# Kernel tuning notes

Hardware: AMD Instinct MI355X
Metric: run time of the kernel (lower is better)

Reference implementation:

```python
import jax, jax.numpy as jnp
import numpy as np

K = 30  # hardcoded top-k in take_top_k_dropout(x, 30, ...)


def _topk_channel_mask(x, k):
    # x: [B, C, H, W]; binary mask with 1 at the top-k |x| channels per pixel.
    B, C, H, W = x.shape
    xa = jnp.abs(x).reshape(B, C, H * W).transpose(0, 2, 1).reshape(B * H * W, C)
    _, idx = jax.lax.top_k(xa, k)  # [BHW, k]
    rows = jnp.arange(B * H * W)[:, None]
    mask = jnp.zeros((B * H * W, C), x.dtype).at[rows, idx].set(1.0)
    return mask.reshape(B, H * W, C).transpose(0, 2, 1).reshape(B, C, H, W)


def _saturation(z, phi, jump):
    # Saturation_activation_per_filter.forward
    l1 = (jnp.sum(jnp.abs(phi), axis=0) + 1e-12).reshape(1, -1, 1, 1)  # [1,C,1,1]
    r = z / l1
    r = 0.5 * (jnp.sign(r - jump) + jnp.sign(r + jump))
    return r * l1


def _conv_transpose(x, w, b, stride):
    # PyTorch ConvTranspose2d(padding=0): w is [in, out, kh, kw]
    k = w.shape[-1]
    wt = jnp.flip(w, (2, 3)).transpose(1, 0, 2, 3)  # -> [out, in, kh, kw]
    y = jax.lax.conv_general_dilated(
        x, wt, window_strides=(1, 1),
        padding=[(k - 1, k - 1), (k - 1, k - 1)],
        lhs_dilation=(stride, stride),
        dimension_numbers=('NCHW', 'OIHW', 'NCHW'))
    return y + b.reshape(1, -1, 1, 1)


def _take_middle(x):
    width = x.shape[-1]
    s = (width - 32) // 2
    return x[:, :, s:s + 32, s:s + 32]


def setup_inputs() -> dict:
    key = jax.random.key(0)
    ks = jax.random.split(key, 9)
    B, C, H, W, D = 128, 500, 16, 16, 192
    return {
        'x': jax.random.normal(ks[0], (B, C, H, W), jnp.float32),
        'phi': jax.random.normal(ks[1], (D, C), jnp.float32),
        'jump': jnp.float32(0.1),
        'w1': jax.random.normal(ks[2], (C, 300, 4, 4), jnp.float32) * 0.02,
        'b1': jax.random.normal(ks[3], (300,), jnp.float32) * 0.02,
        'w2': jax.random.normal(ks[4], (300, 100, 3, 3), jnp.float32) * 0.02,
        'b2': jax.random.normal(ks[5], (100,), jnp.float32) * 0.02,
        'w3': jax.random.normal(ks[6], (100, 3, 3, 3), jnp.float32) * 0.02,
        'b3': jax.random.normal(ks[7], (3,), jnp.float32) * 0.02,
    }


def reference(x, phi, jump, w1, b1, w2, b2, w3, b3):
    # eval mode: dropout(ones) == ones, no training rescalings
    out = x * _topk_channel_mask(x, K)
    out = _saturation(out, phi, jump)
    out = jax.nn.relu(_conv_transpose(out, w1, b1, 2))
    out = jax.nn.relu(_conv_transpose(out, w2, b2, 1))
    out = jax.nn.relu(_conv_transpose(out, w3, b3, 1))
    return _take_middle(out)
```

## Files before the change

kernel.cpp:

```cpp
#include <hip/hip_runtime.h>
#include <stdint.h>

#define B_   128
#define C_   500
#define H_   16
#define P_   256
#define D_   192
#define C1O  300
#define H1   34
#define P1   (H1*H1)
#define C2O  100
#define H2   36
#define P2   (H2*H2)
#define C3O  3
#define H3   38
#define P3   (H3*H3)
#define CROP 3
#define OW_  32
#define KTOP 30

#define NSCAN  1000
#define NL1B   16
#define NTABB  25
#define NPAIR  (B_ * C_)

__device__ __forceinline__ float sgnf(float v){ return (v > 0.f) ? 1.f : ((v < 0.f) ? -1.f : 0.f); }

__device__ __forceinline__ int pat36(int i){
  if (i == 0) return 0;
  if (i == 1) return 1;
  if (i <= 33) return 2;
  if (i == 34) return 3;
  return 4;
}

__global__ __launch_bounds__(256) void k_pre(
    const float* __restrict__ x, const float* __restrict__ phi,
    const float* __restrict__ jumpp, const float* __restrict__ b1,
    const float* __restrict__ w2, const float* __restrict__ b2,
    const float* __restrict__ w3,
    float* __restrict__ l1, float* __restrict__ thr,
    float* __restrict__ tab, float* __restrict__ part,
    float* __restrict__ M){
  const int blk = blockIdx.x;
  const int t = threadIdx.x;
  const int wave = t >> 6, lane = t & 63;

  if (blk < NSCAN){
    const int g = blk * 4 + wave;
    const float* xg = x + (size_t)g * 16 * P_ + lane * 4;
#pragma unroll
    for (int j0 = 0; j0 < 16; j0 += 4){
      float4 v0 = *(const float4*)(xg + (size_t)(j0 + 0) * P_);
      float4 v1 = *(const float4*)(xg + (size_t)(j0 + 1) * P_);
      float4 v2 = *(const float4*)(xg + (size_t)(j0 + 2) * P_);
      float4 v3 = *(const float4*)(xg + (size_t)(j0 + 3) * P_);
      float m0 = fmaxf(fmaxf(fabsf(v0.x), fabsf(v0.y)), fmaxf(fabsf(v0.z), fabsf(v0.w)));
      float m1 = fmaxf(fmaxf(fabsf(v1.x), fabsf(v1.y)), fmaxf(fabsf(v1.z), fabsf(v1.w)));
      float m2 = fmaxf(fmaxf(fabsf(v2.x), fabsf(v2.y)), fmaxf(fabsf(v2.z), fabsf(v2.w)));
      float m3 = fmaxf(fmaxf(fabsf(v3.x), fabsf(v3.y)), fmaxf(fabsf(v3.z), fabsf(v3.w)));
#pragma unroll
      for (int off = 32; off; off >>= 1){
        m0 = fmaxf(m0, __shfl_down(m0, off));
        m1 = fmaxf(m1, __shfl_down(m1, off));
        m2 = fmaxf(m2, __shfl_down(m2, off));
        m3 = fmaxf(m3, __shfl_down(m3, off));
      }
      if (lane == 0)
        *(float4*)(M + g * 16 + j0) = make_float4(m0, m1, m2, m3);
    }
    return;
  }

  if (blk < NSCAN + NL1B){
    __shared__ float red[8][32];
    const int bb = blk - NSCAN;
    const int cl = t & 31, dg = t >> 5;
    const int c = bb * 32 + cl;
    float s = 0.f;
    if (c < C_){
      const int d0 = dg * 24;
#pragma unroll 4
      for (int d = d0; d < d0 + 24; ++d) s += fabsf(phi[d * C_ + c]);
    }
    red[dg][cl] = s;
    __syncthreads();
    if (t < 32){
      int cc = bb * 32 + t;
      if (cc < C_){
        float sum = 1e-12f;
#pragma unroll
        for (int g = 0; g < 8; ++g) sum += red[g][t];
        l1[cc] = sum;
        thr[cc] = jumpp[0] * sum;
      }
    }
    return;
  }

  const int k = blk - (NSCAN + NL1B);
  const int o = k * 4 + wave;
  __shared__ float S[4][9];
  __shared__ float tabR[4][25];
  __shared__ float w3s[4][27];

  for (int i = t; i < 4 * 27; i += 256) w3s[i / 27][i % 27] = w3[(k * 4 + i / 27) * 27 + i % 27];

  {
    float acc[9] = {0,0,0,0,0,0,0,0,0};
    for (int c1 = lane; c1 < C1O; c1 += 64){
      float a1 = fmaxf(b1[c1], 0.f);
      const float* w = w2 + (c1 * C2O + o) * 9;
#pragma unroll
      for (int tap = 0; tap < 9; ++tap) acc[tap] += w[tap] * a1;
    }
#pragma unroll
    for (int tap = 0; tap < 9; ++tap)
      for (int off = 32; off; off >>= 1) acc[tap] += __shfl_down(acc[tap], off);
    if (lane == 0){
#pragma unroll
      for (int tap = 0; tap < 9; ++tap) S[wave][tap] = acc[tap];
    }
  }
  __syncthreads();

  if (lane < 25){
    const int lo5[5] = {0,0,0,1,2}, hi5[5] = {0,1,2,2,2};
    int pr = lane / 5, pc = lane % 5;
    float s = b2[o];
    for (int kh = lo5[pr]; kh <= hi5[pr]; ++kh)
      for (int kw = lo5[pc]; kw <= hi5[pc]; ++kw) s += S[wave][kh * 3 + kw];
    tab[o * 25 + lane] = s;
    tabR[wave][lane] = s;
  }
  __syncthreads();

  for (int pp = 0; pp < 4; ++pp){
    const int pos = pp * 256 + t;
    const int r = pos >> 5, cc = pos & 31;
    const int oh = r + CROP, ow = cc + CROP;
    int ph[3], pw[3];
#pragma unroll
    for (int kk = 0; kk < 3; ++kk){ ph[kk] = pat36(oh - kk); pw[kk] = pat36(ow - kk); }
    float a0 = 0.f, a1v = 0.f, a2v = 0.f;
#pragma unroll
    for (int j = 0; j < 4; ++j){
      const float* tc = tabR[j];
      const float* wc = w3s[j];
#pragma unroll
      for (int kh = 0; kh < 3; ++kh){
        const int prr = ph[kh] * 5;
#pragma unroll
        for (int kw = 0; kw < 3; ++kw){
          float a2 = fmaxf(tc[prr + pw[kw]], 0.f);
          a0  += wc[0 * 9 + kh * 3 + kw] * a2;
          a1v += wc[1 * 9 + kh * 3 + kw] * a2;
          a2v += wc[2 * 9 + kh * 3 + kw] * a2;
        }
      }
    }
    part[(k * 3 + 0) * 1024 + pos] = a0;
    part[(k * 3 + 1) * 1024 + pos] = a1v;
    part[(k * 3 + 2) * 1024 + pos] = a2v;
  }
}

__global__ void k_final(const float* __restrict__ x, const float* __restrict__ l1,
                        const float* __restrict__ jumpp, const float* __restrict__ tab,
                        const float* __restrict__ w1, const float* __restrict__ b1,
                        const float* __restrict__ w2, const float* __restrict__ w3,
                        const float* __restrict__ b3v,
                        const float* __restrict__ part, const float* __restrict__ M,
                        const float* __restrict__ thr,
                        signed char* __restrict__ zq, float* __restrict__ u1,
                        float* __restrict__ u2, float* __restrict__ out, int have){
  const int b = blockIdx.x;
  const int t = threadIdx.x;
  const int wave = t >> 6, lane = t & 63;

  __shared__ unsigned char hot[P_];
  __shared__ unsigned char um[256];
  __shared__ unsigned char d1s[P1];
  __shared__ unsigned char d2s[P2];
  __shared__ int s_any;
  __shared__ float sx[C_];
  __shared__ unsigned char rm[C_];
  __shared__ unsigned long long red[4];
  __shared__ int sel[KTOP];

  if (t == 0) s_any = 0;
  __syncthreads();
  for (int c = t; c < C_; c += 256)
    if (M[b * C_ + c] >= thr[c]) s_any = 1;
  __syncthreads();

  if (!s_any){
    for (int i = t; i < 3 * OW_ * (OW_ / 4); i += 256){
      int o = i >> 8, rr = i & 255;
      int r = rr >> 3, q4 = rr & 7;
      int pos = r * 32 + q4 * 4;
      float bv = b3v[o];
      float4 s = make_float4(bv, bv, bv, bv);
      for (int k = 0; k < NTABB; ++k){
        const float4 v = *(const float4*)(part + ((size_t)(k * 3 + o) << 10) + pos);
        s.x += v.x; s.y += v.y; s.z += v.z; s.w += v.w;
      }
      float4 res;
      res.x = fmaxf(s.x, 0.f);
      res.y = fmaxf(s.y, 0.f);
      res.z = fmaxf(s.z, 0.f);
      res.w = fmaxf(s.w, 0.f);
      *(float4*)(out + ((size_t)(b * 3 + o) * OW_ + r) * OW_ + q4 * 4) = res;
    }
    return;
  }
  if (!have) return;

  {
    const int q = t & 15, cg = t >> 4;
    for (int tile = 0; tile < 4; ++tile){
      unsigned m = 0;
      const int pbase = tile * 64 + 4 * q;
      for (int c = cg; c < C_; c += 16){
        float tc = thr[c];
        const float4 v = *(const float4*)(x + ((size_t)(b * C_ + c)) * P_ + pbase);
        if (fabsf(v.x) >= tc) m |= 1u;
        if (fabsf(v.y) >= tc) m |= 2u;
        if (fabsf(v.z) >= tc) m |= 4u;
        if (fabsf(v.w) >= tc) m |= 8u;
      }
      um[t] = (unsigned char)m;
      __syncthreads();
      if (t < 64){
        const int qq = t >> 2, j = t & 3;
        unsigned mm = 0;
#pragma unroll
        for (int g = 0; g < 16; ++g) mm |= um[g * 16 + qq];
        hot[tile * 64 + t] = (unsigned char)((mm >> j) & 1u);
      }
      __syncthreads();
    }
  }

  const float J = jumpp[0];

  for (int px = 0; px < P_; ++px){
    if (!hot[px]) continue;
    for (int c = t; c < C_; c += 256){ sx[c] = x[(b * C_ + c) * P_ + px]; rm[c] = 0; }
    __syncthreads();
    for (int it = 0; it < KTOP; ++it){
      unsigned long long best = 0ULL;
      for (int c = t; c < C_; c += 256){
        if (!rm[c]){
          unsigned long long key =
            ((unsigned long long)__float_as_uint(fabsf(sx[c])) << 32) |
            (unsigned int)(C_ - 1 - c);
          if (key > best) best = key;
        }
      }
      for (int off = 32; off; off >>= 1){
        unsigned long long o2 = __shfl_down(best, off);
        if (o2 > best) best = o2;
      }
      if ((t & 63) == 0) red[t >> 6] = best;
      __syncthreads();
      if (t == 0){
        unsigned long long mx = red[0];
        for (int wv = 1; wv < 4; ++wv) if (red[wv] > mx) mx = red[wv];
        int idx = C_ - 1 - (int)(mx & 0xffffffffULL);
        sel[it] = idx;
        rm[idx] = 1;
      }
      __syncthreads();
    }
    for (int c = t; c < C_; c += 256) zq[(b * C_ + c) * P_ + px] = 0;
    __syncthreads();
    if (t < KTOP){
      int c = sel[t];
      float r = sx[c] / l1[c];
      float qv = 0.5f * (sgnf(r - J) + sgnf(r + J));
      int code = (int)(2.f * qv);
      if (code) zq[(b * C_ + c) * P_ + px] = (signed char)code;
    }
    __syncthreads();
  }

  for (int p1 = t; p1 < P1; p1 += 256){
    int ih = p1 / H1, iw = p1 - (p1 / H1) * H1;
    int h0 = max(0, (ih - 2) >> 1), h1v = min(H_ - 1, ih >> 1);
    int w0 = max(0, (iw - 2) >> 1), w1v = min(H_ - 1, iw >> 1);
    int any = 0;
    for (int h = h0; h <= h1v; ++h)
      for (int w = w0; w <= w1v; ++w)
        any |= hot[h * H_ + w];
    d1s[p1] = (unsigned char)(any != 0);
  }
  __syncthreads();

  for (int p2 = t; p2 < P2; p2 += 256){
    int oh = p2 / H2, ow = p2 - (p2 / H2) * H2;
    int any = 0;
    for (int kh = 0; kh < 3; ++kh){
      int ih = oh - kh; if (ih < 0 || ih >= H1) continue;
      for (int kw = 0; kw < 3; ++kw){
        int iw = ow - kw; if (iw < 0 || iw >= H1) continue;
        any |= d1s[ih * H1 + iw];
      }
    }
    d2s[p2] = (unsigned char)(any != 0);
  }
  __syncthreads();

  for (int p1 = wave; p1 < P1; p1 += 4){
    if (!d1s[p1]) continue;
    int ih = p1 / H1, iw = p1 - (p1 / H1) * H1;
    float acc[5] = {0,0,0,0,0};
    int h0 = max(0, (ih - 2) >> 1), h1v = min(H_ - 1, ih >> 1);
    int w0 = max(0, (iw - 2) >> 1), w1v = min(H_ - 1, iw >> 1);
    for (int h = h0; h <= h1v; ++h)
      for (int w = w0; w <= w1v; ++w){
        if (!hot[h * H_ + w]) continue;
        int kh = ih - 2 * h, kw = iw - 2 * w;
        const signed char* zp = zq + (size_t)(b * C_) * P_ + h * H_ + w;
        for (int c = 0; c < C_; ++c){
          int code = zp[(size_t)c * P_];
          if (!code) continue;
          float val = 0.5f * (float)code * l1[c];
          const float* wp = w1 + (size_t)(c * C1O) * 16 + kh * 4 + kw;
#pragma unroll
          for (int j = 0; j < 5; ++j){
            int c1 = j * 64 + lane;
            if (c1 < C1O) acc[j] += wp[(size_t)c1 * 16] * val;
          }
        }
      }
#pragma unroll
    for (int j = 0; j < 5; ++j){
      int c1 = j * 64 + lane;
      if (c1 < C1O){
        float bb = b1[c1];
        u1[(size_t)(b * C1O + c1) * P1 + p1] = fmaxf(bb + acc[j], 0.f) - fmaxf(bb, 0.f);
      }
    }
  }
  __syncthreads();

  for (int p2 = wave; p2 < P2; p2 += 4){
    if (!d2s[p2]) continue;
    int oh = p2 / H2, ow = p2 - (p2 / H2) * H2;
    float acc[2] = {0,0};
    for (int kh = 0; kh < 3; ++kh){
      int ih = oh - kh; if (ih < 0 || ih >= H1) continue;
      for (int kw = 0; kw < 3; ++kw){
        int iw = ow - kw; if (iw < 0 || iw >= H1) continue;
        if (!d1s[ih * H1 + iw]) continue;
        const float* up = u1 + (size_t)(b * C1O) * P1 + ih * H1 + iw;
        const float* wb = w2 + kh * 3 + kw;
        for (int c1 = 0; c1 < C1O; ++c1){
          float uv = up[(size_t)c1 * P1];
          if (uv == 0.f) continue;
          const float* wp = wb + (size_t)(c1 * C2O) * 9;
#pragma unroll
          for (int j = 0; j < 2; ++j){
            int c2 = j * 64 + lane;
            if (c2 < C2O) acc[j] += wp[(size_t)c2 * 9] * uv;
          }
        }
      }
    }
    int pr = pat36(oh) * 5 + pat36(ow);
#pragma unroll
    for (int j = 0; j < 2; ++j){
      int c2 = j * 64 + lane;
      if (c2 < C2O){
        float bs = tab[c2 * 25 + pr];
        u2[(size_t)(b * C2O + c2) * P2 + p2] = fmaxf(bs + acc[j], 0.f) - fmaxf(bs, 0.f);
      }
    }
  }
  __syncthreads();

  for (int i = t; i < 3 * OW_ * OW_; i += 256){
    int o = i >> 10, rc = i & 1023;
    int r = rc >> 5, cc = rc & 31;
    int oh = r + CROP, ow = cc + CROP;
    float acc = b3v[o];
    for (int k = 0; k < NTABB; ++k) acc += part[((size_t)(k * 3 + o) << 10) + rc];
    for (int kh = 0; kh < 3; ++kh){
      int ih = oh - kh;
      for (int kw = 0; kw < 3; ++kw){
        int iw = ow - kw;
        if (!d2s[ih * H2 + iw]) continue;
        const float* up = u2 + (size_t)(b * C2O) * P2 + ih * H2 + iw;
        const float* wp = w3 + o * 9 + kh * 3 + kw;
        for (int c2 = 0; c2 < C2O; ++c2){
          float uv = up[(size_t)c2 * P2];
          if (uv != 0.f) acc += wp[c2 * 27] * uv;
        }
      }
    }
    out[((size_t)(b * 3 + o) * OW_ + r) * OW_ + cc] = fmaxf(acc, 0.f);
  }
}

extern "C" void kernel_launch(void* const* d_in, const int* in_sizes, int n_in,
                              void* d_out, int out_size, void* d_ws, size_t ws_size,
                              hipStream_t stream){
  const float* x   = (const float*)d_in[0];
  const float* phi = (const float*)d_in[1];
  const float* jmp = (const float*)d_in[2];
  const float* w1  = (const float*)d_in[3];
  const float* b1  = (const float*)d_in[4];
  const float* w2  = (const float*)d_in[5];
  const float* b2  = (const float*)d_in[6];
  const float* w3  = (const float*)d_in[7];
  const float* b3  = (const float*)d_in[8];
  float* out = (float*)d_out;
  char* ws = (char*)d_ws;

  constexpr size_t OFF_L1   = 0;
  constexpr size_t OFF_THR  = OFF_L1   + 2048;
  constexpr size_t OFF_TAB  = OFF_THR  + 2048;
  constexpr size_t OFF_PART = OFF_TAB  + 10240;
  constexpr size_t OFF_M    = OFF_PART + (size_t)NTABB * 3 * 1024 * 4;
  constexpr size_t OFF_ZQ   = OFF_M    + (size_t)NPAIR * 4;
  constexpr size_t OFF_U1   = OFF_ZQ   + (size_t)B_ * C_ * P_;
  constexpr size_t OFF_U2   = OFF_U1   + (size_t)B_ * C1O * P1 * 4;
  constexpr size_t TOTAL    = OFF_U2   + (size_t)B_ * C2O * P2 * 4;

  float* l1p  = (float*)(ws + OFF_L1);
  float* thrp = (float*)(ws + OFF_THR);
  float* tabp = (float*)(ws + OFF_TAB);
  float* prtp = (float*)(ws + OFF_PART);
  float* Mp   = (float*)(ws + OFF_M);
  signed char* zqp = (signed char*)(ws + OFF_ZQ);
  float* u1p = (float*)(ws + OFF_U1);
  float* u2p = (float*)(ws + OFF_U2);
  int have = (ws_size >= TOTAL) ? 1 : 0;

  k_pre  <<<NSCAN + NL1B + NTABB, 256, 0, stream>>>(x, phi, jmp, b1, w2, b2, w3,
                                                    l1p, thrp, tabp, prtp, Mp);
  k_final<<<B_, 256, 0, stream>>>(x, l1p, jmp, tabp, w1, b1, w2, w3, b3,
                                  prtp, Mp, thrp, zqp, u1p, u2p, out, have);
}
```

Before: 118.5 us.

## Fuse precompute and final kernels into one cooperative launch with grid sync

```diff
diff --git a/kernel.cpp b/kernel.cpp
--- a/kernel.cpp
+++ b/kernel.cpp
@@ -1,5 +1,8 @@
 #include <hip/hip_runtime.h>
+#include <hip/hip_cooperative_groups.h>
 #include <stdint.h>
+
+namespace cg = cooperative_groups;
 
 #define B_   128
 #define C_   500
@@ -22,6 +25,7 @@
 #define NSCAN  1000
 #define NL1B   16
 #define NTABB  25
+#define NGRID  (NSCAN + NL1B + NTABB)
 #define NPAIR  (B_ * C_)
 
 __device__ __forceinline__ float sgnf(float v){ return (v > 0.f) ? 1.f : ((v < 0.f) ? -1.f : 0.f); }
@@ -34,150 +38,26 @@
   return 4;
 }
 
-__global__ __launch_bounds__(256) void k_pre(
+__global__ __launch_bounds__(256, 5) void k_all(
     const float* __restrict__ x, const float* __restrict__ phi,
     const float* __restrict__ jumpp, const float* __restrict__ b1,
     const float* __restrict__ w2, const float* __restrict__ b2,
-    const float* __restrict__ w3,
+    const float* __restrict__ w3, const float* __restrict__ b3v,
+    const float* __restrict__ w1,
     float* __restrict__ l1, float* __restrict__ thr,
     float* __restrict__ tab, float* __restrict__ part,
-    float* __restrict__ M){
+    float* __restrict__ M,
+    signed char* __restrict__ zq, float* __restrict__ u1,
+    float* __restrict__ u2, float* __restrict__ out,
+    int have, int mode){
   const int blk = blockIdx.x;
   const int t = threadIdx.x;
   const int wave = t >> 6, lane = t & 63;
 
-  if (blk < NSCAN){
-    const int g = blk * 4 + wave;
-    const float* xg = x + (size_t)g * 16 * P_ + lane * 4;
-#pragma unroll
-    for (int j0 = 0; j0 < 16; j0 += 4){
-      float4 v0 = *(const float4*)(xg + (size_t)(j0 + 0) * P_);
-      float4 v1 = *(const float4*)(xg + (size_t)(j0 + 1) * P_);
-      float4 v2 = *(const float4*)(xg + (size_t)(j0 + 2) * P_);
-      float4 v3 = *(const float4*)(xg + (size_t)(j0 + 3) * P_);
-      float m0 = fmaxf(fmaxf(fabsf(v0.x), fabsf(v0.y)), fmaxf(fabsf(v0.z), fabsf(v0.w)));
-      float m1 = fmaxf(fmaxf(fabsf(v1.x), fabsf(v1.y)), fmaxf(fabsf(v1.z), fabsf(v1.w)));
-      float m2 = fmaxf(fmaxf(fabsf(v2.x), fabsf(v2.y)), fmaxf(fabsf(v2.z), fabsf(v2.w)));
-      float m3 = fmaxf(fmaxf(fabsf(v3.x), fabsf(v3.y)), fmaxf(fabsf(v3.z), fabsf(v3.w)));
-#pragma unroll
-      for (int off = 32; off; off >>= 1){
-        m0 = fmaxf(m0, __shfl_down(m0, off));
-        m1 = fmaxf(m1, __shfl_down(m1, off));
-        m2 = fmaxf(m2, __shfl_down(m2, off));
-        m3 = fmaxf(m3, __shfl_down(m3, off));
-      }
-      if (lane == 0)
-        *(float4*)(M + g * 16 + j0) = make_float4(m0, m1, m2, m3);
-    }
-    return;
-  }
-
-  if (blk < NSCAN + NL1B){
-    __shared__ float red[8][32];
-    const int bb = blk - NSCAN;
-    const int cl = t & 31, dg = t >> 5;
-    const int c = bb * 32 + cl;
-    float s = 0.f;
-    if (c < C_){
-      const int d0 = dg * 24;
-#pragma unroll 4
-      for (int d = d0; d < d0 + 24; ++d) s += fabsf(phi[d * C_ + c]);
-    }
-    red[dg][cl] = s;
-    __syncthreads();
-    if (t < 32){
-      int cc = bb * 32 + t;
-      if (cc < C_){
-        float sum = 1e-12f;
-#pragma unroll
-        for (int g = 0; g < 8; ++g) sum += red[g][t];
-        l1[cc] = sum;
-        thr[cc] = jumpp[0] * sum;
-      }
-    }
-    return;
-  }
-
-  const int k = blk - (NSCAN + NL1B);
-  const int o = k * 4 + wave;
-  __shared__ float S[4][9];
+  __shared__ float redf[8][32];
+  __shared__ float S4[4][9];
   __shared__ float tabR[4][25];
-  __shared__ float w3s[4][27];
-
-  for (int i = t; i < 4 * 27; i += 256) w3s[i / 27][i % 27] = w3[(k * 4 + i / 27) * 27 + i % 27];
-
-  {
-    float acc[9] = {0,0,0,0,0,0,0,0,0};
-    for (int c1 = lane; c1 < C1O; c1 += 64){
-      float a1 = fmaxf(b1[c1], 0.f);
-      const float* w = w2 + (c1 * C2O + o) * 9;
-#pragma unroll
-      for (int tap = 0; tap < 9; ++tap) acc[tap] += w[tap] * a1;
-    }
-#pragma unroll
-    for (int tap = 0; tap < 9; ++tap)
-      for (int off = 32; off; off >>= 1) acc[tap] += __shfl_down(acc[tap], off);
-    if (lane == 0){
-#pragma unroll
-      for (int tap = 0; tap < 9; ++tap) S[wave][tap] = acc[tap];
-    }
-  }
-  __syncthreads();
-
-  if (lane < 25){
-    const int lo5[5] = {0,0,0,1,2}, hi5[5] = {0,1,2,2,2};
-    int pr = lane / 5, pc = lane % 5;
-    float s = b2[o];
-    for (int kh = lo5[pr]; kh <= hi5[pr]; ++kh)
-      for (int kw = lo5[pc]; kw <= hi5[pc]; ++kw) s += S[wave][kh * 3 + kw];
-    tab[o * 25 + lane] = s;
-    tabR[wave][lane] = s;
-  }
-  __syncthreads();
-
-  for (int pp = 0; pp < 4; ++pp){
-    const int pos = pp * 256 + t;
-    const int r = pos >> 5, cc = pos & 31;
-    const int oh = r + CROP, ow = cc + CROP;
-    int ph[3], pw[3];
-#pragma unroll
-    for (int kk = 0; kk < 3; ++kk){ ph[kk] = pat36(oh - kk); pw[kk] = pat36(ow - kk); }
-    float a0 = 0.f, a1v = 0.f, a2v = 0.f;
-#pragma unroll
-    for (int j = 0; j < 4; ++j){
-      const float* tc = tabR[j];
-      const float* wc = w3s[j];
-#pragma unroll
-      for (int kh = 0; kh < 3; ++kh){
-        const int prr = ph[kh] * 5;
-#pragma unroll
-        for (int kw = 0; kw < 3; ++kw){
-          float a2 = fmaxf(tc[prr + pw[kw]], 0.f);
-          a0  += wc[0 * 9 + kh * 3 + kw] * a2;
-          a1v += wc[1 * 9 + kh * 3 + kw] * a2;
-          a2v += wc[2 * 9 + kh * 3 + kw] * a2;
-        }
-      }
-    }
-    part[(k * 3 + 0) * 1024 + pos] = a0;
-    part[(k * 3 + 1) * 1024 + pos] = a1v;
-    part[(k * 3 + 2) * 1024 + pos] = a2v;
-  }
-}
-
-__global__ void k_final(const float* __restrict__ x, const float* __restrict__ l1,
-                        const float* __restrict__ jumpp, const float* __restrict__ tab,
-                        const float* __restrict__ w1, const float* __restrict__ b1,
-                        const float* __restrict__ w2, const float* __restrict__ w3,
-                        const float* __restrict__ b3v,
-                        const float* __restrict__ part, const float* __restrict__ M,
-                        const float* __restrict__ thr,
-                        signed char* __restrict__ zq, float* __restrict__ u1,
-                        float* __restrict__ u2, float* __restrict__ out, int have){
-  const int b = blockIdx.x;
-  const int t = threadIdx.x;
-  const int wave = t >> 6, lane = t & 63;
-
+  __shared__ float w3s4[4][27];
   __shared__ unsigned char hot[P_];
   __shared__ unsigned char um[256];
   __shared__ unsigned char d1s[P1];
@@ -185,8 +65,126 @@
   __shared__ int s_any;
   __shared__ float sx[C_];
   __shared__ unsigned char rm[C_];
-  __shared__ unsigned long long red[4];
+  __shared__ unsigned long long redu[4];
   __shared__ int sel[KTOP];
+
+  if (mode != 2){
+    if (blk < NSCAN){
+      const int g = blk * 4 + wave;
+      const float* xg = x + (size_t)g * 16 * P_ + lane * 4;
+#pragma unroll
+      for (int j0 = 0; j0 < 16; j0 += 4){
+        float4 v0 = *(const float4*)(xg + (size_t)(j0 + 0) * P_);
+        float4 v1 = *(const float4*)(xg + (size_t)(j0 + 1) * P_);
+        float4 v2 = *(const float4*)(xg + (size_t)(j0 + 2) * P_);
+        float4 v3 = *(const float4*)(xg + (size_t)(j0 + 3) * P_);
+        float m0 = fmaxf(fmaxf(fabsf(v0.x), fabsf(v0.y)), fmaxf(fabsf(v0.z), fabsf(v0.w)));
+        float m1 = fmaxf(fmaxf(fabsf(v1.x), fabsf(v1.y)), fmaxf(fabsf(v1.z), fabsf(v1.w)));
+        float m2 = fmaxf(fmaxf(fabsf(v2.x), fabsf(v2.y)), fmaxf(fabsf(v2.z), fabsf(v2.w)));
+        float m3 = fmaxf(fmaxf(fabsf(v3.x), fabsf(v3.y)), fmaxf(fabsf(v3.z), fabsf(v3.w)));
+#pragma unroll
+        for (int off = 32; off; off >>= 1){
+          m0 = fmaxf(m0, __shfl_down(m0, off));
+          m1 = fmaxf(m1, __shfl_down(m1, off));
+          m2 = fmaxf(m2, __shfl_down(m2, off));
+          m3 = fmaxf(m3, __shfl_down(m3, off));
+        }
+        if (lane == 0)
+          *(float4*)(M + g * 16 + j0) = make_float4(m0, m1, m2, m3);
+      }
+    } else if (blk < NSCAN + NL1B){
+      const int bb = blk - NSCAN;
+      const int cl = t & 31, dg = t >> 5;
+      const int c = bb * 32 + cl;
+      float s = 0.f;
+      if (c < C_){
+        const int d0 = dg * 24;
+#pragma unroll 4
+        for (int d = d0; d < d0 + 24; ++d) s += fabsf(phi[d * C_ + c]);
+      }
+      redf[dg][cl] = s;
+      __syncthreads();
+      if (t < 32){
+        int cc = bb * 32 + t;
+        if (cc < C_){
+          float sum = 1e-12f;
+#pragma unroll
+          for (int g = 0; g < 8; ++g) sum += redf[g][t];
+          l1[cc] = sum;
+          thr[cc] = jumpp[0] * sum;
+        }
+      }
+    } else {
+      const int k = blk - (NSCAN + NL1B);
+      const int o = k * 4 + wave;
+      for (int i = t; i < 4 * 27; i += 256)
+        w3s4[i / 27][i % 27] = w3[(k * 4 + i / 27) * 27 + i % 27];
+      {
+        float acc[9] = {0,0,0,0,0,0,0,0,0};
+        for (int c1 = lane; c1 < C1O; c1 += 64){
+          float a1 = fmaxf(b1[c1], 0.f);
+          const float* w = w2 + (c1 * C2O + o) * 9;
+#pragma unroll
+          for (int tap = 0; tap < 9; ++tap) acc[tap] += w[tap] * a1;
+        }
+#pragma unroll
+        for (int tap = 0; tap < 9; ++tap)
+          for (int off = 32; off; off >>= 1) acc[tap] += __shfl_down(acc[tap], off);
+        if (lane == 0){
+#pragma unroll
+          for (int tap = 0; tap < 9; ++tap) S4[wave][tap] = acc[tap];
+        }
+      }
+      __syncthreads();
+      if (lane < 25){
+        const int lo5[5] = {0,0,0,1,2}, hi5[5] = {0,1,2,2,2};
+        int pr = lane / 5, pc = lane % 5;
+        float s = b2[o];
+        for (int kh = lo5[pr]; kh <= hi5[pr]; ++kh)
+          for (int kw = lo5[pc]; kw <= hi5[pc]; ++kw) s += S4[wave][kh * 3 + kw];
+        tab[o * 25 + lane] = s;
+        tabR[wave][lane] = s;
+      }
+      __syncthreads();
+      for (int pp = 0; pp < 4; ++pp){
+        const int pos = pp * 256 + t;
+        const int r = pos >> 5, cc = pos & 31;
+        const int oh = r + CROP, ow = cc + CROP;
+        int ph[3], pw[3];
+#pragma unroll
+        for (int kk = 0; kk < 3; ++kk){ ph[kk] = pat36(oh - kk); pw[kk] = pat36(ow - kk); }
+        float a0 = 0.f, a1v = 0.f, a2v = 0.f;
+#pragma unroll
+        for (int j = 0; j < 4; ++j){
+          const float* tc = tabR[j];
+          const float* wc = w3s4[j];
+#pragma unroll
+          for (int kh = 0; kh < 3; ++kh){
+            const int prr = ph[kh] * 5;
+#pragma unroll
+            for (int kw = 0; kw < 3; ++kw){
+              float a2 = fmaxf(tc[prr + pw[kw]], 0.f);
+              a0  += wc[0 * 9 + kh * 3 + kw] * a2;
+              a1v += wc[1 * 9 + kh * 3 + kw] * a2;
+              a2v += wc[2 * 9 + kh * 3 + kw] * a2;
+            }
+          }
+        }
+        part[(k * 3 + 0) * 1024 + pos] = a0;
+        part[(k * 3 + 1) * 1024 + pos] = a1v;
+        part[(k * 3 + 2) * 1024 + pos] = a2v;
+      }
+    }
+  }
+
+  if (mode == 0){
+    __threadfence();
+    cg::this_grid().sync();
+  }
+  if (mode == 1) return;
+
+  const int b = blk;
+  if (b >= B_) return;
 
   if (t == 0) s_any = 0;
   __syncthreads();
@@ -217,11 +215,11 @@
   if (!have) return;
 
   {
-    const int q = t & 15, cg = t >> 4;
+    const int q = t & 15, cg2 = t >> 4;
     for (int tile = 0; tile < 4; ++tile){
       unsigned m = 0;
       const int pbase = tile * 64 + 4 * q;
-      for (int c = cg; c < C_; c += 16){
+      for (int c = cg2; c < C_; c += 16){
         float tc = thr[c];
         const float4 v = *(const float4*)(x + ((size_t)(b * C_ + c)) * P_ + pbase);
         if (fabsf(v.x) >= tc) m |= 1u;
@@ -262,11 +260,11 @@
         unsigned long long o2 = __shfl_down(best, off);
         if (o2 > best) best = o2;
       }
-      if ((t & 63) == 0) red[t >> 6] = best;
+      if ((t & 63) == 0) redu[t >> 6] = best;
       __syncthreads();
       if (t == 0){
-        unsigned long long mx = red[0];
-        for (int wv = 1; wv < 4; ++wv) if (red[wv] > mx) mx = red[wv];
+        unsigned long long mx = redu[0];
+        for (int wv = 1; wv < 4; ++wv) if (redu[wv] > mx) mx = redu[wv];
         int idx = C_ - 1 - (int)(mx & 0xffffffffULL);
         sel[it] = idx;
         rm[idx] = 1;
@@ -438,8 +436,22 @@
   float* u2p = (float*)(ws + OFF_U2);
   int have = (ws_size >= TOTAL) ? 1 : 0;
 
-  k_pre  <<<NSCAN + NL1B + NTABB, 256, 0, stream>>>(x, phi, jmp, b1, w2, b2, w3,
-                                                    l1p, thrp, tabp, prtp, Mp);
-  k_final<<<B_, 256, 0, stream>>>(x, l1p, jmp, tabp, w1, b1, w2, w3, b3,
-                                  prtp, Mp, thrp, zqp, u1p, u2p, out, have);
+  int mode0 = 0;
+  void* args[] = {
+    (void*)&x, (void*)&phi, (void*)&jmp, (void*)&b1, (void*)&w2, (void*)&b2,
+    (void*)&w3, (void*)&b3, (void*)&w1,
+    (void*)&l1p, (void*)&thrp, (void*)&tabp, (void*)&prtp, (void*)&Mp,
+    (void*)&zqp, (void*)&u1p, (void*)&u2p, (void*)&out,
+    (void*)&have, (void*)&mode0
+  };
+  hipError_t e = hipLaunchCooperativeKernel((const void*)k_all, dim3(NGRID), dim3(256),
+                                            args, 0, stream);
+  if (e != hipSuccess){
+    hipLaunchKernelGGL(k_all, dim3(NGRID), dim3(256), 0, stream,
+                       x, phi, jmp, b1, w2, b2, w3, b3, w1,
+                       l1p, thrp, tabp, prtp, Mp, zqp, u1p, u2p, out, have, 1);
+    hipLaunchKernelGGL(k_all, dim3(B_), dim3(256), 0, stream,
+                       x, phi, jmp, b1, w2, b2, w3, b3, w1,
+                       l1p, thrp, tabp, prtp, Mp, zqp, u1p, u2p, out, have, 2);
+  }
 }
```

After: 363.8 us. +207.1%, slower.
